# Kernel optimization log

Measured on AMD Instinct MI355X. Metric: run time of the kernel, lower is better.

## Reference

```python
import jax, jax.numpy as jnp
import numpy as np

B, N, D = 8, 65536, 3
K = 64                 # num_centers
NPOINT = 4096
M = NPOINT // K * 2    # max_neighbors = 128
S = NPOINT // K        # fps samples per group = 64
NITER = 10             # KMeans default Niter


def _sqdist(src, dst):
    # ||s||^2 + ||d||^2 - 2 s.d   (same math as (s-d)^2 sum, GEMM form)
    s2 = (src ** 2).sum(-1)[:, :, None]          # [B,N,1]
    d2 = (dst ** 2).sum(-1)[:, None, :]          # [B,1,K]
    return s2 + d2 - 2.0 * jnp.einsum('bnd,bkd->bnk', src, dst)


def _kmeans(x):
    Bb, Nn, Dd = x.shape
    c = x[:, :K, :]
    bidx = jnp.arange(Bb)[:, None]               # broadcast with cl [B,N]
    for _ in range(NITER):
        cl = jnp.argmin(_sqdist(x, c), axis=2)   # [B,N] cluster codes
        c = jnp.zeros((Bb, K, Dd), x.dtype).at[bidx, cl].add(x)
        ncl = jnp.zeros((Bb, K), x.dtype).at[bidx, cl].add(1.0)
        c = c / ncl[:, :, None]
    return c


def _query_neighbor(x, centers):
    dist = _sqdist(x, centers)                   # [B,N,K]
    negd = -jnp.transpose(dist, (0, 2, 1))       # [B,K,N]
    _, nidx = jax.lax.top_k(negd, M)             # M nearest points per center
    bidx = jnp.arange(x.shape[0])[:, None, None]
    return x[bidx, nidx]                         # [B,K,M,3]


def _batch_fps(xyz, farthest0):
    # xyz: [B,G,Nn,3]; sequential farthest-point sampling per group
    Bb, G, Nn, _ = xyz.shape
    dist0 = jnp.full((Bb, G, Nn), 1e10, xyz.dtype)

    def step(carry, _):
        distance, farthest = carry
        centroid = jnp.take_along_axis(xyz, farthest[:, :, None, None], axis=2)  # [B,G,1,3]
        d = ((xyz - centroid) ** 2).sum(-1)       # [B,G,Nn]
        distance = jnp.minimum(distance, d)
        new_far = jnp.argmax(distance, -1).astype(farthest.dtype)
        return (distance, new_far), farthest      # store index BEFORE update

    _, idx = jax.lax.scan(step, (dist0, farthest0), None, length=S)
    idx = jnp.transpose(idx, (1, 2, 0))           # [B,G,S]
    idx3 = jnp.broadcast_to(idx[..., None], idx.shape + (3,))
    new_xyz = jnp.take_along_axis(xyz, idx3, axis=2)  # [B,G,S,3]
    return new_xyz.reshape(Bb, G * S, 3)


def setup_inputs() -> dict:
    key = jax.random.key(0)
    k1, k2 = jax.random.split(key)
    x = jax.random.normal(k1, (B, N, D), dtype=jnp.float32)
    farthest0 = jax.random.randint(k2, (B, K), 0, M, dtype=jnp.int32)
    return {"x": x, "farthest0": farthest0}


def reference(x, farthest0):
    centers = _kmeans(x)                  # [B,K,3]
    neighbor = _query_neighbor(x, centers)  # [B,K,M,3]
    new_xyz = _batch_fps(neighbor, farthest0)  # [B, NPOINT, 3]
    return new_xyz, centers
```

## Files before the change

kernel.cpp:

```cpp
#include <hip/hip_runtime.h>
#include <stdint.h>

#pragma clang fp contract(off)

#define B 8
#define N 65536
#define KC 64
#define M 128
#define S 64
#define NITER 10
#define HPAD 257
#define SAMPLE 8192
#define SCAP 2048
#define CAPG 3072
#define WCAP 512
#define CSTRIDE 32
#define NCHK 64
#define URANGE 16384
#define UNR (N / URANGE)
#define UPPT 64
#define UBATCH 1024

using u32 = unsigned int;
using u64 = unsigned long long;
using u16 = unsigned short;

__device__ __forceinline__ float sq3(float a, float b, float c) {
  return __fadd_rn(__fadd_rn(__fmul_rn(a, a), __fmul_rn(b, b)), __fmul_rn(c, c));
}
__device__ __forceinline__ float dot3(float x0, float x1, float x2,
                                      float c0, float c1, float c2) {
  return __fadd_rn(__fadd_rn(__fmul_rn(x0, c0), __fmul_rn(x1, c1)), __fmul_rn(x2, c2));
}
__device__ __forceinline__ float distf(float s2, float d2, float dt) {
  return __fsub_rn(__fadd_rn(s2, d2), __fmul_rn(2.0f, dt));
}
__device__ __forceinline__ u32 fkey(float f) {
  u32 u = __float_as_uint(f);
  return (u & 0x80000000u) ? ~u : (u | 0x80000000u);
}


__global__ void k_init_centers(const float* __restrict__ x, float* __restrict__ centers) {
  int i = blockIdx.x * blockDim.x + threadIdx.x;
  if (i >= B * KC * 3) return;
  int b = i / (KC * 3);
  int r = i % (KC * 3);
  centers[i] = x[(size_t)b * N * 3 + r];
}

__global__ __launch_bounds__(256)
void k_assign(const float* __restrict__ x, const float* __restrict__ centers,
              unsigned char* __restrict__ cl) {
  __shared__ float4 cs[KC];
  int g = blockIdx.x;
  int b = g & 7;
  int chunk = g >> 3;
  int t = threadIdx.x;
  if (t < KC) {
    float a0 = centers[(b * KC + t) * 3 + 0];
    float a1 = centers[(b * KC + t) * 3 + 1];
    float a2 = centers[(b * KC + t) * 3 + 2];
    cs[t] = make_float4(a0, a1, a2, sq3(a0, a1, a2));
  }
  __syncthreads();
  int q = chunk * 256 + t;
  const float4* xb4 = (const float4*)(x + (size_t)b * N * 3);
  float4 A = xb4[3 * q], Bv = xb4[3 * q + 1], C = xb4[3 * q + 2];
  float p0x = A.x, p0y = A.y, p0z = A.z;
  float p1x = A.w, p1y = Bv.x, p1z = Bv.y;
  float p2x = Bv.z, p2y = Bv.w, p2z = C.x;
  float p3x = C.y, p3y = C.z, p3z = C.w;
  float s0 = sq3(p0x, p0y, p0z);
  float s1 = sq3(p1x, p1y, p1z);
  float s2 = sq3(p2x, p2y, p2z);
  float s3 = sq3(p3x, p3y, p3z);
  float inf = __int_as_float(0x7f800000);
  float b0 = inf, b1 = inf, b2 = inf, b3 = inf;
  int i0 = 0, i1 = 0, i2 = 0, i3 = 0;
  for (int k = 0; k < KC; ++k) {
    float4 cc = cs[k];
    float d0 = distf(s0, cc.w, dot3(p0x, p0y, p0z, cc.x, cc.y, cc.z));
    float d1 = distf(s1, cc.w, dot3(p1x, p1y, p1z, cc.x, cc.y, cc.z));
    float d2 = distf(s2, cc.w, dot3(p2x, p2y, p2z, cc.x, cc.y, cc.z));
    float d3 = distf(s3, cc.w, dot3(p3x, p3y, p3z, cc.x, cc.y, cc.z));
    if (d0 < b0) { b0 = d0; i0 = k; }
    if (d1 < b1) { b1 = d1; i1 = k; }
    if (d2 < b2) { b2 = d2; i2 = k; }
    if (d3 < b3) { b3 = d3; i3 = k; }
  }
  *(u32*)(cl + (size_t)b * N + 4 * q) =
      (u32)i0 | ((u32)i1 << 8) | ((u32)i2 << 16) | ((u32)i3 << 24);
}

__global__ __launch_bounds__(256)
void k_cluster_update(const float* __restrict__ x, const unsigned char* __restrict__ cl,
                      float* __restrict__ centers) {
  __shared__ u16 midx[URANGE];
  __shared__ float bcoord[2][3][UBATCH + 1];
  __shared__ int woff[4];
  int g = blockIdx.x;
  int bk = ((g & 7) << 6) | (g >> 3);
  int b = bk >> 6, k = bk & 63;
  int t = threadIdx.x, lane = t & 63, wid = t >> 6;
  const unsigned char* clb = cl + (size_t)b * N;
  const float* xb = x + (size_t)b * N * 3;
  float acc = 0.f;
  int cntAll = 0;

  for (int r = 0; r < UNR; ++r) {
    u32 words[16];
    {
      const uint4* cp = (const uint4*)(clb + (size_t)r * URANGE) + t * 4;
#pragma unroll
      for (int j = 0; j < 4; ++j) {
        uint4 v = cp[j];
        words[4 * j] = v.x; words[4 * j + 1] = v.y;
        words[4 * j + 2] = v.z; words[4 * j + 3] = v.w;
      }
    }
    int m = 0;
#pragma unroll
    for (int j = 0; j < 16; ++j) {
      u32 w4 = words[j];
      m += (int)((w4 & 255u) == (u32)k) + (int)(((w4 >> 8) & 255u) == (u32)k)
         + (int)(((w4 >> 16) & 255u) == (u32)k) + (int)(((w4 >> 24) & 255u) == (u32)k);
    }
    int incl = m;
#pragma unroll
    for (int o = 1; o < 64; o <<= 1) {
      int u = __shfl_up(incl, o);
      if (lane >= o) incl += u;
    }
    if (lane == 63) woff[wid] = incl;
    __syncthreads();
    int w0 = woff[0], w1 = woff[1], w2v = woff[2], w3 = woff[3];
    int tot = w0 + w1 + w2v + w3;
    int wbase = (wid > 0 ? w0 : 0) + (wid > 1 ? w1 : 0) + (wid > 2 ? w2v : 0);
    int off = wbase + incl - m;
    int base = t * UPPT;
#pragma unroll
    for (int j = 0; j < 16; ++j) {
      u32 w4 = words[j];
#pragma unroll
      for (int s = 0; s < 4; ++s)
        if (((w4 >> (8 * s)) & 255u) == (u32)k) midx[off++] = (u16)(base + 4 * j + s);
    }
    __syncthreads();
    int rbase = r * URANGE;
    int nb = (tot + UBATCH - 1) / UBATCH;
    if (t >= 64 && nb > 0) {
      int bn = min(UBATCH, tot);
      for (int i = t - 64; i < bn; i += 192) {
        int li = rbase + (int)midx[i];
        bcoord[0][0][i] = xb[3 * li];
        bcoord[0][1][i] = xb[3 * li + 1];
        bcoord[0][2][i] = xb[3 * li + 2];
      }
    }
    __syncthreads();
    for (int z = 0; z < nb; ++z) {
      if (t >= 64) {
        if (z + 1 < nb) {
          int bo = (z + 1) * UBATCH;
          int bn = min(UBATCH, tot - bo);
          int pb = (z + 1) & 1;
          for (int i = t - 64; i < bn; i += 192) {
            int li = rbase + (int)midx[bo + i];
            bcoord[pb][0][i] = xb[3 * li];
            bcoord[pb][1][i] = xb[3 * li + 1];
            bcoord[pb][2][i] = xb[3 * li + 2];
          }
        }
      } else if (t < 3) {
        const float* bb = &bcoord[z & 1][t][0];
        int bn = min(UBATCH, tot - z * UBATCH);
#pragma unroll 8
        for (int i = 0; i < bn; ++i) acc = __fadd_rn(acc, bb[i]);
      }
      __syncthreads();
    }
    cntAll += tot;
  }
  if (t < 3) centers[bk * 3 + t] = __fdiv_rn(acc, (float)cntAll);
}

__global__ __launch_bounds__(256)
void k_thresh(const float* __restrict__ x, const float* __restrict__ centers,
              u32* __restrict__ thr, u32* __restrict__ cnt) {
  __shared__ u32 whist[4 * HPAD];
  __shared__ int sv[256];
  __shared__ u32 skeys[SCAP];
  __shared__ float4 scen;
  __shared__ u32 sSel;
  __shared__ int sNeed, sCntBin, sNum;
  int g = blockIdx.x;
  int bk = ((g & 7) << 6) | (g >> 3);
  int b = bk >> 6;
  int t = threadIdx.x, wid = t >> 6;
  if (t == 0) {
    float c0 = centers[bk * 3], c1 = centers[bk * 3 + 1], c2 = centers[bk * 3 + 2];
    scen = make_float4(c0, c1, c2, sq3(c0, c1, c2));
    cnt[bk * CSTRIDE] = 0;
    sNum = 0;
  }
  for (int i = t; i < 4 * HPAD; i += 256) whist[i] = 0;
  __syncthreads();
  float c0 = scen.x, c1 = scen.y, c2 = scen.z, d2 = scen.w;
  const float2* xb2 = (const float2*)(x + (size_t)b * N * 3);

  for (int p = t; p < SAMPLE / 2; p += 256) {
    float2 A = xb2[3 * p], Bv = xb2[3 * p + 1], C = xb2[3 * p + 2];
    float d0 = distf(sq3(A.x, A.y, Bv.x), d2, dot3(A.x, A.y, Bv.x, c0, c1, c2));
    float d1 = distf(sq3(Bv.y, C.x, C.y), d2, dot3(Bv.y, C.x, C.y, c0, c1, c2));
    atomicAdd(&whist[wid * HPAD + (fkey(d0) >> 24)], 1u);
    atomicAdd(&whist[wid * HPAD + (fkey(d1) >> 24)], 1u);
  }
  __syncthreads();
  int own = (int)(whist[0 * HPAD + t] + whist[1 * HPAD + t] +
                  whist[2 * HPAD + t] + whist[3 * HPAD + t]);
  sv[t] = own;
  __syncthreads();
  for (int off = 1; off < 256; off <<= 1) {
    int add = (t >= off) ? sv[t - off] : 0;
    __syncthreads();
    sv[t] += add;
    __syncthreads();
  }
  if (sv[t] >= M && sv[t] - own < M) {
    sSel = (u32)t; sNeed = M - (sv[t] - own); sCntBin = own;
  }
  __syncthreads();
  u32 selByte = sSel;
  int need = sNeed;
  int cntBin = sCntBin;
  u32 prefix = selByte << 24;

  if (cntBin <= SCAP) {
    for (int p = t; p < SAMPLE / 2; p += 256) {
      float2 A = xb2[3 * p], Bv = xb2[3 * p + 1], C = xb2[3 * p + 2];
      float d0 = distf(sq3(A.x, A.y, Bv.x), d2, dot3(A.x, A.y, Bv.x, c0, c1, c2));
      float d1 = distf(sq3(Bv.y, C.x, C.y), d2, dot3(Bv.y, C.x, C.y, c0, c1, c2));
      u32 k0 = fkey(d0), k1 = fkey(d1);
      if ((k0 >> 24) == selByte) skeys[atomicAdd(&sNum, 1)] = k0;
      if ((k1 >> 24) == selByte) skeys[atomicAdd(&sNum, 1)] = k1;
    }
    __syncthreads();
    int ne = sNum;
    for (int sh = 16; sh >= 0; sh -= 8) {
      whist[t] = 0;
      __syncthreads();
      for (int i = t; i < ne; i += 256) {
        u32 kkk = skeys[i];
        if ((kkk >> (sh + 8)) == (prefix >> (sh + 8)))
          atomicAdd(&whist[(kkk >> sh) & 255u], 1u);
      }
      __syncthreads();
      int own2 = (int)whist[t];
      sv[t] = own2;
      __syncthreads();
      for (int off = 1; off < 256; off <<= 1) {
        int add = (t >= off) ? sv[t - off] : 0;
        __syncthreads();
        sv[t] += add;
        __syncthreads();
      }
      if (sv[t] >= need && sv[t] - own2 < need) {
        sSel = prefix | ((u32)t << sh);
        sNeed = need - (sv[t] - own2);
      }
      __syncthreads();
      prefix = sSel; need = sNeed;
      __syncthreads();
    }
    if (t == 0) thr[bk] = prefix;
  } else {
    if (t == 0) thr[bk] = prefix | 0x00FFFFFFu;
  }
}

__global__ __launch_bounds__(256)
void k_scatter_test(const float* __restrict__ x, const float* __restrict__ centers,
                    const u32* __restrict__ thr, u32* __restrict__ cnt,
                    u32* __restrict__ cand) {
  __shared__ float4 cs[KC];
  __shared__ u32 lthr[KC];
  __shared__ u64 wm0[4][KC], wm1[4][KC];
  __shared__ u32 wbase[4][KC];
  int g = blockIdx.x;
  int b = g & 7;
  int chunk = g >> 3;
  int t = threadIdx.x, lane = t & 63, wid = t >> 6;
  if (t < KC) {
    float a0 = centers[(b * KC + t) * 3 + 0];
    float a1 = centers[(b * KC + t) * 3 + 1];
    float a2 = centers[(b * KC + t) * 3 + 2];
    cs[t] = make_float4(a0, a1, a2, sq3(a0, a1, a2));
    lthr[t] = thr[b * KC + t];
  }
  __syncthreads();
  int pr = chunk * 256 + t;
  const float2* xb2 = (const float2*)(x + (size_t)b * N * 3);
  float2 A = xb2[3 * pr], Bv = xb2[3 * pr + 1], C = xb2[3 * pr + 2];
  float s20 = sq3(A.x, A.y, Bv.x);
  float s21 = sq3(Bv.y, C.x, C.y);
  u32 n0 = 2 * pr, n1 = 2 * pr + 1;
  u64 ltm = ((u64)1 << lane) - 1;

  for (int k = 0; k < KC; ++k) {
    float4 cc = cs[k];
    float d0 = distf(s20, cc.w, dot3(A.x, A.y, Bv.x, cc.x, cc.y, cc.z));
    float d1 = distf(s21, cc.w, dot3(Bv.y, C.x, C.y, cc.x, cc.y, cc.z));
    u64 m0 = __ballot(fkey(d0) <= lthr[k]);
    u64 m1 = __ballot(fkey(d1) <= lthr[k]);
    if (lane == 0) { wm0[wid][k] = m0; wm1[wid][k] = m1; }
  }
  __syncthreads();
  if (t < KC) {
    u32 pc[4];
    u32 total = 0;
#pragma unroll
    for (int w = 0; w < 4; ++w) {
      pc[w] = (u32)(__popcll(wm0[w][t]) + __popcll(wm1[w][t]));
      total += pc[w];
    }
    u32 base = (total > 0) ? atomicAdd(&cnt[(b * KC + t) * CSTRIDE], total) : 0u;
#pragma unroll
    for (int w = 0; w < 4; ++w) { wbase[w][t] = base; base += pc[w]; }
  }
  __syncthreads();
  u64 mybit = (u64)1 << lane;
  for (int k = 0; k < KC; ++k) {
    u64 m0 = wm0[wid][k], m1 = wm1[wid][k];
    if ((m0 | m1) == 0) continue;
    u32 wb = wbase[wid][k];
    u32* cb = cand + (size_t)(b * KC + k) * CAPG;
    if (m0 & mybit) {
      u32 pos = wb + (u32)__popcll(m0 & ltm);
      if (pos < CAPG) cb[pos] = n0;
    }
    if (m1 & mybit) {
      u32 pos = wb + (u32)__popcll(m0) + (u32)__popcll(m1 & ltm);
      if (pos < CAPG) cb[pos] = n1;
    }
  }
}

__global__ __launch_bounds__(256)
void k_topk_sort(const float* __restrict__ x, const float* __restrict__ centers,
                 const u32* __restrict__ cnt, const u32* __restrict__ cand,
                 float* __restrict__ neighbor) {
  __shared__ u64 candList[CAPG];
  __shared__ u32 hist[256];
  __shared__ u64 wbuf[WCAP];
  __shared__ u64 lessList[M];
  __shared__ u32 eqList[256];
  __shared__ u32 sSel;
  __shared__ int sNeed;
  __shared__ int cntW, cntLess, cntEq;
  __shared__ float4 scen;
  int g = blockIdx.x;
  int bk = ((g & 7) << 6) | (g >> 3);
  int b = bk >> 6;
  int t = threadIdx.x, lane = t & 63, wid = t >> 6;
  if (t == 0) {
    float c0 = centers[bk * 3], c1 = centers[bk * 3 + 1], c2 = centers[bk * 3 + 2];
    scen = make_float4(c0, c1, c2, sq3(c0, c1, c2));
    cntW = 0;
  }
  __syncthreads();
  float c0 = scen.x, c1 = scen.y, c2 = scen.z, d2 = scen.w;
  const float* xb = x + (size_t)b * N * 3;
  int cc = (int)cnt[bk * CSTRIDE];

  if (cc <= CAPG) {
    const u32* cb = cand + (size_t)bk * CAPG;
    for (int i = t; i < cc; i += 256) {
      u32 n = cb[i];
      float x0 = xb[n * 3], x1 = xb[n * 3 + 1], x2 = xb[n * 3 + 2];
      float d = distf(sq3(x0, x1, x2), d2, dot3(x0, x1, x2, c0, c1, c2));
      candList[i] = ((u64)fkey(d) << 32) | n;
    }
    __syncthreads();
    u32 prefix = 0;
    int need = M;
    for (int r = 3; r >= 0; --r) {
      int sh = r * 8;
      hist[t] = 0;
      __syncthreads();
      for (int i = t; i < cc; i += 256) {
        u32 key = (u32)(candList[i] >> 32);
        bool ok = (r == 3) || ((key >> (sh + 8)) == (prefix >> (sh + 8)));
        if (ok) atomicAdd(&hist[(key >> sh) & 255u], 1u);
      }
      __syncthreads();
      if (wid == 0) {
        u32 h0 = hist[4 * lane + 0], h1 = hist[4 * lane + 1];
        u32 h2 = hist[4 * lane + 2], h3 = hist[4 * lane + 3];
        u32 lsum = h0 + h1 + h2 + h3;
        u32 incl = lsum;
#pragma unroll
        for (int o = 1; o < 64; o <<= 1) {
          u32 u = __shfl_up(incl, o);
          if (lane >= o) incl += u;
        }
        u32 excl = incl - lsum;
        if ((int)excl < need && need <= (int)incl) {
          u32 hh[4] = {h0, h1, h2, h3};
          u32 cum = excl; int bin = -1; u32 bc = 0;
#pragma unroll
          for (int j = 0; j < 4; ++j) {
            if (bin < 0 && (int)(cum + hh[j]) >= need) { bin = 4 * lane + j; bc = cum; }
            cum += hh[j];
          }
          sSel = prefix | ((u32)bin << sh);
          sNeed = need - (int)bc;
        }
      }
      __syncthreads();
      prefix = sSel; need = sNeed;
      __syncthreads();
    }
    u32 K128 = prefix;
    for (int i = t; i < cc; i += 256) {
      u64 e = candList[i];
      if ((u32)(e >> 32) <= K128) {
        int p = atomicAdd(&cntW, 1);
        if (p < WCAP) wbuf[p] = e;
      }
    }
    __syncthreads();
    int wcnt2 = cntW;
    if (wcnt2 <= WCAP) {
      for (int i = t; i < WCAP; i += 256) if (i >= wcnt2) wbuf[i] = ~0ull;
      __syncthreads();
      for (int ksz = 2; ksz <= WCAP; ksz <<= 1) {
        for (int j = ksz >> 1; j > 0; j >>= 1) {
          for (int idx = t; idx < WCAP; idx += 256) {
            int ixj = idx ^ j;
            if (ixj > idx) {
              u64 a = wbuf[idx], bb = wbuf[ixj];
              bool up = ((idx & ksz) == 0);
              if (up ? (a > bb) : (a < bb)) { wbuf[idx] = bb; wbuf[ixj] = a; }
            }
          }
          __syncthreads();
        }
      }
      if (t < M) {
        int idx = (int)(wbuf[t] & 0xFFFFFFFFu);
        size_t src = ((size_t)b * N + idx) * 3;
        size_t dst = ((size_t)bk * M + t) * 3;
        neighbor[dst]     = x[src];
        neighbor[dst + 1] = x[src + 1];
        neighbor[dst + 2] = x[src + 2];
      }
      return;
    }
  }

  if (t == 0) { cntLess = 0; cntEq = 0; }
  __syncthreads();
  u32 prefix = 0;
  int need = M;
  for (int r = 3; r >= 0; --r) {
    for (int i = t; i < 256; i += 256) hist[i] = 0;
    __syncthreads();
    int sh = r * 8;
    for (int n = t; n < N; n += 256) {
      float x0 = xb[n * 3], x1 = xb[n * 3 + 1], x2 = xb[n * 3 + 2];
      float d = distf(sq3(x0, x1, x2), d2, dot3(x0, x1, x2, c0, c1, c2));
      u32 key = fkey(d);
      bool ok = (r == 3) || ((key >> (sh + 8)) == (prefix >> (sh + 8)));
      if (ok) atomicAdd(&hist[(key >> sh) & 255u], 1u);
    }
    __syncthreads();
    if (t == 0) {
      int cum = 0;
      for (int bin = 0; bin < 256; ++bin) {
        int ccv = (int)hist[bin];
        if (cum + ccv >= need) { sSel = prefix | ((u32)bin << sh); sNeed = need - cum; break; }
        cum += ccv;
      }
    }
    __syncthreads();
    prefix = sSel; need = sNeed;
    __syncthreads();
  }
  u32 K128 = prefix;

  for (int n = t; n < N; n += 256) {
    float x0 = xb[n * 3], x1 = xb[n * 3 + 1], x2 = xb[n * 3 + 2];
    float d = distf(sq3(x0, x1, x2), d2, dot3(x0, x1, x2, c0, c1, c2));
    u32 key = fkey(d);
    if (key < K128) {
      int p = atomicAdd(&cntLess, 1);
      if (p < M) lessList[p] = ((u64)key << 32) | (u32)n;
    } else if (key == K128) {
      int p = atomicAdd(&cntEq, 1);
      if (p < 256) eqList[p] = (u32)n;
    }
  }
  __syncthreads();
  int nl = cntLess;
  int ne2 = cntEq;
  for (int i = t; i < M; i += 256) if (i >= nl) lessList[i] = ~0ull;
  for (int i = t; i < 256; i += 256) if (i >= ne2) eqList[i] = 0xFFFFFFFFu;
  __syncthreads();

  for (int ksz = 2; ksz <= M; ksz <<= 1) {
    for (int j = ksz >> 1; j > 0; j >>= 1) {
      for (int idx = t; idx < M; idx += 256) {
        int ixj = idx ^ j;
        if (ixj > idx) {
          u64 a = lessList[idx], bb = lessList[ixj];
          bool up = ((idx & ksz) == 0);
          if (up ? (a > bb) : (a < bb)) { lessList[idx] = bb; lessList[ixj] = a; }
        }
      }
      __syncthreads();
    }
  }
  for (int ksz = 2; ksz <= 256; ksz <<= 1) {
    for (int j = ksz >> 1; j > 0; j >>= 1) {
      for (int idx = t; idx < 256; idx += 256) {
        int ixj = idx ^ j;
        if (ixj > idx) {
          u32 a = eqList[idx], bb = eqList[ixj];
          bool up = ((idx & ksz) == 0);
          if (up ? (a > bb) : (a < bb)) { eqList[idx] = bb; eqList[ixj] = a; }
        }
      }
      __syncthreads();
    }
  }

  if (t < M) {
    int idx = (t < nl) ? (int)(lessList[t] & 0xFFFFFFFFu) : (int)eqList[t - nl];
    size_t src = ((size_t)b * N + idx) * 3;
    size_t dst = ((size_t)bk * M + t) * 3;
    neighbor[dst]     = x[src];
    neighbor[dst + 1] = x[src + 1];
    neighbor[dst + 2] = x[src + 2];
  }
}

__global__ __launch_bounds__(64)
void k_fps(const float* __restrict__ neighbor, const int* __restrict__ farthest0,
           const float* __restrict__ centers, float* __restrict__ out) {
  __shared__ float4 pts[M];
  int bg = blockIdx.x;
  int b = bg >> 6, g = bg & 63;
  int t = threadIdx.x;
  {
    int i = bg * 64 + t;
    if (i < B * KC * 3) out[B * 4096 * 3 + i] = centers[i];
  }
  const float* nb = neighbor + (size_t)bg * M * 3;
  float ax = nb[6 * t],     ay = nb[6 * t + 1], az = nb[6 * t + 2];
  float bx = nb[6 * t + 3], by = nb[6 * t + 4], bz = nb[6 * t + 5];
  pts[2 * t]     = make_float4(ax, ay, az, 0.f);
  pts[2 * t + 1] = make_float4(bx, by, bz, 0.f);
  int far = farthest0[bg];
  float dist0 = 1e10f, dist1 = 1e10f;
  __syncthreads();
  float* ob = out + ((size_t)b * 4096 + g * 64) * 3;
  for (int s = 0; s < S; ++s) {
    if ((far >> 1) == t) {
      if (far & 1) { ob[3 * s] = bx; ob[3 * s + 1] = by; ob[3 * s + 2] = bz; }
      else         { ob[3 * s] = ax; ob[3 * s + 1] = ay; ob[3 * s + 2] = az; }
    }
    float4 cc = pts[far];
    float d0 = sq3(__fsub_rn(ax, cc.x), __fsub_rn(ay, cc.y), __fsub_rn(az, cc.z));
    float d1 = sq3(__fsub_rn(bx, cc.x), __fsub_rn(by, cc.y), __fsub_rn(bz, cc.z));
    dist0 = fminf(dist0, d0);
    dist1 = fminf(dist1, d1);
    u64 k0 = ((u64)__float_as_uint(dist0) << 32) | (u32)(M - 1 - 2 * t);
    u64 k1 = ((u64)__float_as_uint(dist1) << 32) | (u32)(M - 2 - 2 * t);
    u64 key = (k0 > k1) ? k0 : k1;
#pragma unroll
    for (int off = 1; off < 64; off <<= 1) {
      u64 o = __shfl_xor(key, off);
      if (o > key) key = o;
    }
    far = M - 1 - (int)(key & 0xFFFFFFFFu);
  }
}

extern "C" void kernel_launch(void* const* d_in, const int* in_sizes, int n_in,
                              void* d_out, int out_size, void* d_ws, size_t ws_size,
                              hipStream_t stream) {
  const float* x = (const float*)d_in[0];
  const int* farthest0 = (const int*)d_in[1];
  float* out = (float*)d_out;

  char* w = (char*)d_ws;
  float* centers  = (float*)(w);
  unsigned char* cl = (unsigned char*)(w + 8192);
  u32* thr        = (u32*)(w + 8192 + 524288);
  u32* cnt        = (u32*)(w + 8192 + 524288 + 4096);
  float* neighbor = (float*)(w + 8192 + 524288 + 4096 + 65536);
  u32* cand       = (u32*)(w + 8192 + 524288 + 4096 + 65536 + 786432);

  k_init_centers<<<6, 256, 0, stream>>>(x, centers);
  for (int it = 0; it < NITER; ++it) {
    k_assign<<<B * NCHK, 256, 0, stream>>>(x, centers, cl);
    k_cluster_update<<<B * KC, 256, 0, stream>>>(x, cl, centers);
  }
  k_thresh<<<B * KC, 256, 0, stream>>>(x, centers, thr, cnt);
  k_scatter_test<<<B * NCHK * 2, 256, 0, stream>>>(x, centers, thr, cnt, cand);
  k_topk_sort<<<B * KC, 256, 0, stream>>>(x, centers, cnt, cand, neighbor);
  k_fps<<<B * KC, M / 2, 0, stream>>>(neighbor, farthest0, centers, out);
}
```

Before: 519.8 us.

## Overlap next-range cluster scan with accumulation in a dedicated-wave pipeline

The cluster-update kernel now runs 320 threads: wave 0 only does the serial coordinate accumulation, while waves 1-4 compact cluster-member indices into per-wave segments and stage coordinates. Scanning the next 16K-point range now overlaps with accumulating the last batch of the current range, which removes barriers and exposed scan latency per range. Staging uses float3 loads and stores absolute indices, so the rbase offset is dropped. The cost is a segment lookup per staged element and more threads per block, which may lower occupancy.

```diff
diff --git a/kernel.cpp b/kernel.cpp
--- a/kernel.cpp
+++ b/kernel.cpp
@@ -18,7 +18,7 @@
 #define NCHK 64
 #define URANGE 16384
 #define UNR (N / URANGE)
-#define UPPT 64
+#define SEG 4096
 #define UBATCH 1024
 
 using u32 = unsigned int;
@@ -93,12 +93,12 @@
       (u32)i0 | ((u32)i1 << 8) | ((u32)i2 << 16) | ((u32)i3 << 24);
 }
 
-__global__ __launch_bounds__(256)
+__global__ __launch_bounds__(320)
 void k_cluster_update(const float* __restrict__ x, const unsigned char* __restrict__ cl,
                       float* __restrict__ centers) {
-  __shared__ u16 midx[URANGE];
+  __shared__ u16 midx[4][SEG];
   __shared__ float bcoord[2][3][UBATCH + 1];
-  __shared__ int woff[4];
+  __shared__ int wcnt[4];
   int g = blockIdx.x;
   int bk = ((g & 7) << 6) | (g >> 3);
   int b = bk >> 6, k = bk & 63;
@@ -108,81 +108,104 @@
   float acc = 0.f;
   int cntAll = 0;
 
+#define SCAN(RR)                                                            \
+  {                                                                         \
+    int w_ = wid - 1;                                                       \
+    int base_ = (RR) * URANGE + w_ * SEG + lane * 64;                       \
+    const uint4* cp_ = (const uint4*)(clb + base_);                         \
+    u32 words_[16];                                                         \
+    _Pragma("unroll")                                                       \
+    for (int j_ = 0; j_ < 4; ++j_) {                                        \
+      uint4 v_ = cp_[j_];                                                   \
+      words_[4 * j_] = v_.x; words_[4 * j_ + 1] = v_.y;                     \
+      words_[4 * j_ + 2] = v_.z; words_[4 * j_ + 3] = v_.w;                 \
+    }                                                                       \
+    int m_ = 0;                                                             \
+    _Pragma("unroll")                                                       \
+    for (int j_ = 0; j_ < 16; ++j_) {                                       \
+      u32 w4_ = words_[j_];                                                 \
+      m_ += (int)((w4_ & 255u) == (u32)k) + (int)(((w4_ >> 8) & 255u) == (u32)k) \
+          + (int)(((w4_ >> 16) & 255u) == (u32)k) + (int)(((w4_ >> 24) & 255u) == (u32)k); \
+    }                                                                       \
+    int incl_ = m_;                                                         \
+    _Pragma("unroll")                                                       \
+    for (int o_ = 1; o_ < 64; o_ <<= 1) {                                   \
+      int u_ = __shfl_up(incl_, o_);                                        \
+      if (lane >= o_) incl_ += u_;                                          \
+    }                                                                       \
+    int off_ = incl_ - m_;                                                  \
+    _Pragma("unroll")                                                       \
+    for (int j_ = 0; j_ < 16; ++j_) {                                       \
+      u32 w4_ = words_[j_];                                                 \
+      _Pragma("unroll")                                                     \
+      for (int s_ = 0; s_ < 4; ++s_)                                        \
+        if (((w4_ >> (8 * s_)) & 255u) == (u32)k)                           \
+          midx[w_][off_++] = (u16)(base_ + 4 * j_ + s_);                    \
+    }                                                                       \
+    if (lane == 63) wcnt[w_] = incl_;                                       \
+  }
+
+#define STAGE(BO, BN, PB)                                                   \
+  {                                                                         \
+    int c0_ = wcnt[0], c1_ = wcnt[1], c2_ = wcnt[2];                        \
+    int st_ = t - 64;                                                       \
+    for (int i_ = st_; i_ < (BN); i_ += 256) {                              \
+      int fi_ = (BO) + i_;                                                  \
+      int seg_, off_;                                                       \
+      if (fi_ < c0_) { seg_ = 0; off_ = fi_; }                              \
+      else if (fi_ < c0_ + c1_) { seg_ = 1; off_ = fi_ - c0_; }             \
+      else if (fi_ < c0_ + c1_ + c2_) { seg_ = 2; off_ = fi_ - c0_ - c1_; } \
+      else { seg_ = 3; off_ = fi_ - c0_ - c1_ - c2_; }                      \
+      int li_ = (int)midx[seg_][off_];                                      \
+      float3 v_ = *(const float3*)(xb + 3 * (size_t)li_);                   \
+      bcoord[PB][0][i_] = v_.x;                                             \
+      bcoord[PB][1][i_] = v_.y;                                             \
+      bcoord[PB][2][i_] = v_.z;                                             \
+    }                                                                       \
+  }
+
+  if (wid > 0) SCAN(0);
+  __syncthreads();
+  int tot = wcnt[0] + wcnt[1] + wcnt[2] + wcnt[3];
+  if (wid > 0) STAGE(0, min(UBATCH, tot), 0);
+  __syncthreads();
+
   for (int r = 0; r < UNR; ++r) {
-    u32 words[16];
-    {
-      const uint4* cp = (const uint4*)(clb + (size_t)r * URANGE) + t * 4;
-#pragma unroll
-      for (int j = 0; j < 4; ++j) {
-        uint4 v = cp[j];
-        words[4 * j] = v.x; words[4 * j + 1] = v.y;
-        words[4 * j + 2] = v.z; words[4 * j + 3] = v.w;
-      }
-    }
-    int m = 0;
-#pragma unroll
-    for (int j = 0; j < 16; ++j) {
-      u32 w4 = words[j];
-      m += (int)((w4 & 255u) == (u32)k) + (int)(((w4 >> 8) & 255u) == (u32)k)
-         + (int)(((w4 >> 16) & 255u) == (u32)k) + (int)(((w4 >> 24) & 255u) == (u32)k);
-    }
-    int incl = m;
-#pragma unroll
-    for (int o = 1; o < 64; o <<= 1) {
-      int u = __shfl_up(incl, o);
-      if (lane >= o) incl += u;
-    }
-    if (lane == 63) woff[wid] = incl;
-    __syncthreads();
-    int w0 = woff[0], w1 = woff[1], w2v = woff[2], w3 = woff[3];
-    int tot = w0 + w1 + w2v + w3;
-    int wbase = (wid > 0 ? w0 : 0) + (wid > 1 ? w1 : 0) + (wid > 2 ? w2v : 0);
-    int off = wbase + incl - m;
-    int base = t * UPPT;
-#pragma unroll
-    for (int j = 0; j < 16; ++j) {
-      u32 w4 = words[j];
-#pragma unroll
-      for (int s = 0; s < 4; ++s)
-        if (((w4 >> (8 * s)) & 255u) == (u32)k) midx[off++] = (u16)(base + 4 * j + s);
-    }
-    __syncthreads();
-    int rbase = r * URANGE;
     int nb = (tot + UBATCH - 1) / UBATCH;
-    if (t >= 64 && nb > 0) {
-      int bn = min(UBATCH, tot);
-      for (int i = t - 64; i < bn; i += 192) {
-        int li = rbase + (int)midx[i];
-        bcoord[0][0][i] = xb[3 * li];
-        bcoord[0][1][i] = xb[3 * li + 1];
-        bcoord[0][2][i] = xb[3 * li + 2];
-      }
-    }
-    __syncthreads();
+    if (nb == 0) nb = 1;
     for (int z = 0; z < nb; ++z) {
-      if (t >= 64) {
+      int bn = tot - z * UBATCH;
+      if (bn > UBATCH) bn = UBATCH;
+      if (wid == 0) {
+        if (lane < 3 && bn > 0) {
+          const float* bb = &bcoord[z & 1][lane][0];
+#pragma unroll 8
+          for (int i = 0; i < bn; ++i) acc = __fadd_rn(acc, bb[i]);
+        }
+      } else {
         if (z + 1 < nb) {
           int bo = (z + 1) * UBATCH;
-          int bn = min(UBATCH, tot - bo);
-          int pb = (z + 1) & 1;
-          for (int i = t - 64; i < bn; i += 192) {
-            int li = rbase + (int)midx[bo + i];
-            bcoord[pb][0][i] = xb[3 * li];
-            bcoord[pb][1][i] = xb[3 * li + 1];
-            bcoord[pb][2][i] = xb[3 * li + 2];
-          }
+          int bn2 = tot - bo;
+          if (bn2 > UBATCH) bn2 = UBATCH;
+          STAGE(bo, bn2, (z + 1) & 1);
+        } else if (r + 1 < UNR) {
+          SCAN(r + 1);
         }
-      } else if (t < 3) {
-        const float* bb = &bcoord[z & 1][t][0];
-        int bn = min(UBATCH, tot - z * UBATCH);
-#pragma unroll 8
-        for (int i = 0; i < bn; ++i) acc = __fadd_rn(acc, bb[i]);
       }
       __syncthreads();
     }
     cntAll += tot;
-  }
-  if (t < 3) centers[bk * 3 + t] = __fdiv_rn(acc, (float)cntAll);
+    if (r + 1 < UNR) {
+      int ntot = wcnt[0] + wcnt[1] + wcnt[2] + wcnt[3];
+      if (wid > 0) STAGE(0, min(UBATCH, ntot), 0);
+      __syncthreads();
+      tot = ntot;
+    }
+  }
+  if (wid == 0 && lane < 3)
+    centers[bk * 3 + lane] = __fdiv_rn(acc, (float)cntAll);
+#undef SCAN
+#undef STAGE
 }
 
 __global__ __launch_bounds__(256)
@@ -605,7 +628,7 @@
   k_init_centers<<<6, 256, 0, stream>>>(x, centers);
   for (int it = 0; it < NITER; ++it) {
     k_assign<<<B * NCHK, 256, 0, stream>>>(x, centers, cl);
-    k_cluster_update<<<B * KC, 256, 0, stream>>>(x, cl, centers);
+    k_cluster_update<<<B * KC, 320, 0, stream>>>(x, cl, centers);
   }
   k_thresh<<<B * KC, 256, 0, stream>>>(x, centers, thr, cnt);
   k_scatter_test<<<B * NCHK * 2, 256, 0, stream>>>(x, centers, thr, cnt, cand);
```

New measurement: 625.7 us. 20.4% more time.
